# Performance work log

Hardware: AMD Instinct MI355X
Metric: run time of the kernel (lower is better)

The kernel has to match this reference:

```python
import jax, jax.numpy as jnp
import numpy as np
from jax.ops import segment_sum, segment_max

N, E, IN_DIM, HID, HEADS, B, ACTIONS = 16384, 262144, 512, 256, 4, 64, 32
NEG_SLOPE = 0.2  # PyG GATConv default leaky-relu slope


def setup_inputs() -> dict:
    key = jax.random.key(0)
    ks = jax.random.split(key, 12)
    x = jax.random.normal(ks[0], (N, IN_DIM), dtype=jnp.float32)
    edge_index = jax.random.randint(ks[1], (2, E), 0, N, dtype=jnp.int64)
    batch = jnp.sort(jax.random.randint(ks[2], (N,), 0, B, dtype=jnp.int64))
    s = 0.05
    return {
        "x": x,
        "edge_index": edge_index,
        "batch": batch,
        # SAGEConv: lin_l (neighbors, with bias) + lin_r (root, no bias)
        "sage_w_l": jax.random.normal(ks[3], (IN_DIM, HID), dtype=jnp.float32) * s,
        "sage_b_l": jnp.zeros((HID,), dtype=jnp.float32),
        "sage_w_r": jax.random.normal(ks[4], (IN_DIM, HID), dtype=jnp.float32) * s,
        # GATConv: shared lin, per-head attention vectors, output bias (concat=False)
        "gat_w": jax.random.normal(ks[5], (HID, HEADS * HID), dtype=jnp.float32) * s,
        "gat_att_src": jax.random.normal(ks[6], (HEADS, HID), dtype=jnp.float32) * s,
        "gat_att_dst": jax.random.normal(ks[7], (HEADS, HID), dtype=jnp.float32) * s,
        "gat_b": jnp.zeros((HID,), dtype=jnp.float32),
        # action head
        "head_w": jax.random.normal(ks[8], (HID, ACTIONS), dtype=jnp.float32) * s,
        "head_b": jnp.zeros((ACTIONS,), dtype=jnp.float32),
    }


def reference(x, edge_index, batch, sage_w_l, sage_b_l, sage_w_r,
              gat_w, gat_att_src, gat_att_dst, gat_b, head_w, head_b):
    src, dst = edge_index[0], edge_index[1]

    # ---- SAGEConv (mean aggregation): lin_l(mean_j x_j) + lin_r(x_i) ----
    agg = segment_sum(x[src], dst, num_segments=N)                 # [N, IN_DIM]
    deg = segment_sum(jnp.ones((E,), x.dtype), dst, num_segments=N)
    mean_nbr = agg / jnp.maximum(deg, 1.0)[:, None]
    h = mean_nbr @ sage_w_l + sage_b_l + x @ sage_w_r              # [N, HID]
    h = jax.nn.relu(h)
    # dropout is identity at inference (training=False)

    # ---- GATConv (adds self-loops, concat=False -> head average) ----
    loop = jnp.arange(N, dtype=src.dtype)
    si = jnp.concatenate([src, loop])                              # [E2]
    di = jnp.concatenate([dst, loop])
    g = (h @ gat_w).reshape(N, HEADS, HID)                         # [N, H, C]
    a_src = jnp.einsum('nhc,hc->nh', g, gat_att_src)               # [N, H]
    a_dst = jnp.einsum('nhc,hc->nh', g, gat_att_dst)
    logits = jax.nn.leaky_relu(a_src[si] + a_dst[di], NEG_SLOPE)   # [E2, H]
    m = segment_max(logits, di, num_segments=N)                    # per-target max
    ex = jnp.exp(logits - m[di])
    denom = segment_sum(ex, di, num_segments=N)
    alpha = ex / denom[di]                                         # [E2, H]
    out = segment_sum(g[si] * alpha[:, :, None], di, num_segments=N)  # [N, H, C]
    out = jax.nn.relu(out.mean(axis=1) + gat_b)                    # [N, HID]

    # ---- global mean pool + action head ----
    pooled = segment_sum(out, batch, num_segments=B)
    cnt = segment_sum(jnp.ones((N,), out.dtype), batch, num_segments=B)
    pooled = pooled / jnp.maximum(cnt, 1.0)[:, None]               # [B, HID]
    return pooled @ head_w + head_b                                # [B, ACTIONS]
```

## Files before the change

### kernel.cpp

```cpp
#include <hip/hip_runtime.h>
#include <math.h>

#define N_NODES 16384
#define N_EDGES 262144
#define IN_DIM  512
#define HID     256
#define HEADS   4
#define NBATCH  64
#define ACTIONS 32
#define NEG_SLOPE 0.2f

typedef __attribute__((ext_vector_type(8))) short short8;
typedef __attribute__((ext_vector_type(4))) float f32x4;

__device__ __forceinline__ float lrelu(float v) { return v > 0.f ? v : NEG_SLOPE * v; }

__device__ __forceinline__ unsigned short bf16_rne(float f) {
    union { float f; unsigned int u; } x; x.f = f;
    unsigned int u = x.u;
    unsigned int r = (u + 0x7FFFu + ((u >> 16) & 1u)) >> 16;
    return (unsigned short)r;
}

__device__ __forceinline__ float bf16_to_f32(unsigned short s) {
    union { unsigned int u; float f; } x; x.u = (unsigned int)s << 16;
    return x.f;
}

__device__ __forceinline__ float4 bf4_to_f4(ushort4 u) {
    return make_float4(bf16_to_f32(u.x), bf16_to_f32(u.y), bf16_to_f32(u.z), bf16_to_f32(u.w));
}

__device__ __forceinline__ void async_copy16(const unsigned short* g, unsigned short* l) {
    __builtin_amdgcn_global_load_lds(
        (const __attribute__((address_space(1))) unsigned int*)g,
        (__attribute__((address_space(3))) unsigned int*)l, 16, 0, 0);
}

#define NB_WLR   1024
#define NB_WSTK  1024
#define NB_WATT  8
#define NB_DEG   1024
#define NB_XCONV 4096
#define NB_SETUP (NB_WLR + NB_WSTK + NB_WATT + NB_DEG + NB_XCONV)

__global__ __launch_bounds__(256) void setup_kernel(
        const float* __restrict__ wl, const float* __restrict__ wr, unsigned short* __restrict__ bt1,
        const float* __restrict__ gat_w, unsigned short* __restrict__ bt2,
        const float* __restrict__ att_src, const float* __restrict__ att_dst, float* __restrict__ watt,
        const int* __restrict__ ei, int* __restrict__ deg,
        const float* __restrict__ x, unsigned short* __restrict__ xb) {
    int bid = blockIdx.x, tid = threadIdx.x;
    if (bid < NB_WLR) {
        int idx = bid * 256 + tid;
        int j = idx >> 9;
        int k = idx & 511;
        float v = (j < HID) ? wl[k * HID + j] : wr[k * HID + (j - HID)];
        bt1[idx] = bf16_rne(v);
    } else if (bid < NB_WLR + NB_WSTK) {
        int idx = (bid - NB_WLR) * 256 + tid;
        int c = idx >> 10;
        int r = idx & 1023;
        int h = r >> 8;
        int k = r & 255;
        bt2[idx] = bf16_rne(gat_w[(size_t)k * (HEADS * HID) + h * HID + c]);
    } else if (bid < NB_WLR + NB_WSTK + NB_WATT) {
        int j = bid - NB_WLR - NB_WSTK;
        int c = tid;
        int hh = j & 3;
        const float* att = (j < 4) ? (att_src + hh * HID) : (att_dst + hh * HID);
        float s = 0.f;
        for (int cc = 0; cc < HID; cc++)
            s += gat_w[(size_t)c * (HEADS * HID) + hh * HID + cc] * att[cc];
        watt[j * HID + c] = s;
    } else if (bid < NB_WLR + NB_WSTK + NB_WATT + NB_DEG) {
        int e = (bid - NB_WLR - NB_WSTK - NB_WATT) * 256 + tid;
        if (e < N_EDGES) atomicAdd(&deg[ei[N_EDGES + e]], 1);
    } else {
        size_t idx = (size_t)(bid - NB_WLR - NB_WSTK - NB_WATT - NB_DEG) * 2048 + (size_t)tid * 8;
        float4 a0 = *(const float4*)(x + idx);
        float4 a1 = *(const float4*)(x + idx + 4);
        short8 p;
        p[0] = (short)bf16_rne(a0.x); p[1] = (short)bf16_rne(a0.y);
        p[2] = (short)bf16_rne(a0.z); p[3] = (short)bf16_rne(a0.w);
        p[4] = (short)bf16_rne(a1.x); p[5] = (short)bf16_rne(a1.y);
        p[6] = (short)bf16_rne(a1.z); p[7] = (short)bf16_rne(a1.w);
        *(short8*)(xb + idx) = p;
    }
}

__global__ __launch_bounds__(256) void scan_kernel(const int* __restrict__ deg,
                                                   int* __restrict__ row_start,
                                                   int* __restrict__ pos) {
    int t = threadIdx.x;
    int lane = t & 63, wv = t >> 6;
    int base = t * 64;
    int4 buf[16];
    int sum = 0;
#pragma unroll
    for (int i = 0; i < 16; i++) {
        buf[i] = ((const int4*)(deg + base))[i];
        sum += buf[i].x + buf[i].y + buf[i].z + buf[i].w;
    }
    int v = sum;
#pragma unroll
    for (int off = 1; off < 64; off <<= 1) {
        int u = __shfl_up(v, off);
        if (lane >= off) v += u;
    }
    __shared__ int wsum[4];
    if (lane == 63) wsum[wv] = v;
    __syncthreads();
    int wbase = 0;
    for (int w0 = 0; w0 < wv; w0++) wbase += wsum[w0];
    int run = wbase + v - sum;
#pragma unroll
    for (int i = 0; i < 16; i++) {
        int4 b = buf[i];
        int4 o;
        o.x = run; run += b.x;
        o.y = run; run += b.y;
        o.z = run; run += b.z;
        o.w = run; run += b.w;
        ((int4*)(row_start + base))[i] = o;
        ((int4*)(pos + base))[i] = o;
    }
    if (t == 255) row_start[N_NODES] = run;
}

__global__ void fill_kernel(const int* __restrict__ ei, int* __restrict__ pos,
                            int* __restrict__ col) {
    int e = blockIdx.x * 256 + threadIdx.x;
    if (e < N_EDGES) {
        int s = ei[e];
        int d = ei[N_EDGES + e];
        int p = atomicAdd(&pos[d], 1);
        col[p] = s;
    }
}

#define BK 32

__global__ __launch_bounds__(256) void gemm1_kernel(const unsigned short* __restrict__ Ab,
                                                    const unsigned short* __restrict__ Bt,
                                                    unsigned short* __restrict__ Cb,
                                                    int Nn, int K) {
    __shared__ __align__(16) unsigned short As[2][2][64 * BK];
    __shared__ __align__(16) unsigned short Bs[2][2][128 * BK];

    int tid  = threadIdx.x;
    int wv   = tid >> 6;
    int lane = tid & 63;
    int m0 = blockIdx.y * 64;
    int n0 = blockIdx.x * 128;
    int wm = (wv & 1) * 32;
    int wn = (wv >> 1) * 64;

    int srow = tid >> 2;
    int scol = (tid & 3) * 8;
    const unsigned short* Ag  = Ab + (size_t)(m0 + srow) * K + scol;
    const unsigned short* Bg0 = Bt + (size_t)(n0 + srow) * K + scol;
    const unsigned short* Bg1 = Bt + (size_t)(n0 + 64 + srow) * K + scol;

    int fr = lane & 15;
    int fk = (lane >> 4) * 8;
    f32x4 acc[2][4] = {};

#pragma unroll
    for (int s = 0; s < 2; s++) {
        int ko = s * BK;
        async_copy16(Ag + ko,      &As[0][s][wv * 512]);
        async_copy16(Bg0 + ko,     &Bs[0][s][wv * 512]);
        async_copy16(Bg1 + ko,     &Bs[0][s][2048 + wv * 512]);
    }
    __syncthreads();

    int cur = 0;
    for (int kt = 0; kt < K; kt += 2 * BK) {
        int nxt = kt + 2 * BK;
        bool pf = nxt < K;
        if (pf) {
#pragma unroll
            for (int s = 0; s < 2; s++) {
                int ko = nxt + s * BK;
                async_copy16(Ag + ko,  &As[cur ^ 1][s][wv * 512]);
                async_copy16(Bg0 + ko, &Bs[cur ^ 1][s][wv * 512]);
                async_copy16(Bg1 + ko, &Bs[cur ^ 1][s][2048 + wv * 512]);
            }
        }

#pragma unroll
        for (int s = 0; s < 2; s++) {
            short8 af[2], bf[4];
#pragma unroll
            for (int mi = 0; mi < 2; mi++)
                af[mi] = *(const short8*)&As[cur][s][(wm + mi * 16 + fr) * BK + fk];
#pragma unroll
            for (int ni = 0; ni < 4; ni++)
                bf[ni] = *(const short8*)&Bs[cur][s][(wn + ni * 16 + fr) * BK + fk];
#pragma unroll
            for (int mi = 0; mi < 2; mi++)
#pragma unroll
                for (int ni = 0; ni < 4; ni++)
                    acc[mi][ni] = __builtin_amdgcn_mfma_f32_16x16x32_bf16(af[mi], bf[ni], acc[mi][ni], 0, 0, 0);
        }
        __syncthreads();
        cur ^= 1;
    }

    int cr = (lane >> 4) * 4;
    int cc = lane & 15;
#pragma unroll
    for (int mi = 0; mi < 2; mi++) {
#pragma unroll
        for (int ni = 0; ni < 4; ni++) {
            int gc = n0 + wn + ni * 16 + cc;
#pragma unroll
            for (int r = 0; r < 4; r++) {
                int gr = m0 + wm + mi * 16 + cr + r;
                Cb[(size_t)gr * Nn + gc] = bf16_rne(acc[mi][ni][r]);
            }
        }
    }
}

__global__ __launch_bounds__(256) void gemm2_pool_kernel(const unsigned short* __restrict__ A,
                                                         const unsigned short* __restrict__ Bt,
                                                         const int* __restrict__ batch,
                                                         const float* __restrict__ bias,
                                                         float scale,
                                                         float* __restrict__ pooled,
                                                         int Nn, int K) {
    __shared__ __align__(16) unsigned short As[2][2][64 * BK];
    __shared__ __align__(16) unsigned short Bs[2][2][64 * BK];
    __shared__ int bsh[64];

    int tid  = threadIdx.x;
    int wv   = tid >> 6;
    int lane = tid & 63;
    int m0 = blockIdx.y * 64;
    int n0 = blockIdx.x * 64;
    int wm = (wv & 1) * 32;
    int wn = (wv >> 1) * 32;

    if (tid < 64) bsh[tid] = batch[m0 + tid];

    int srow = tid >> 2;
    int scol = (tid & 3) * 8;
    const unsigned short* Ag = A  + (size_t)(m0 + srow) * K + scol;
    const unsigned short* Bg = Bt + (size_t)(n0 + srow) * K + scol;

    int fr = lane & 15;
    int fk = (lane >> 4) * 8;
    f32x4 acc[2][2] = {};

#pragma unroll
    for (int s = 0; s < 2; s++) {
        int ko = s * BK;
        async_copy16(Ag + ko, &As[0][s][wv * 512]);
        async_copy16(Bg + ko, &Bs[0][s][wv * 512]);
    }
    __syncthreads();

    int cur = 0;
    for (int kt = 0; kt < K; kt += 2 * BK) {
        int nxt = kt + 2 * BK;
        bool pf = nxt < K;
        if (pf) {
#pragma unroll
            for (int s = 0; s < 2; s++) {
                int ko = nxt + s * BK;
                async_copy16(Ag + ko, &As[cur ^ 1][s][wv * 512]);
                async_copy16(Bg + ko, &Bs[cur ^ 1][s][wv * 512]);
            }
        }

#pragma unroll
        for (int s = 0; s < 2; s++) {
            short8 af[2], bf[2];
#pragma unroll
            for (int mi = 0; mi < 2; mi++)
                af[mi] = *(const short8*)&As[cur][s][(wm + mi * 16 + fr) * BK + fk];
#pragma unroll
            for (int ni = 0; ni < 2; ni++)
                bf[ni] = *(const short8*)&Bs[cur][s][(wn + ni * 16 + fr) * BK + fk];
#pragma unroll
            for (int mi = 0; mi < 2; mi++)
#pragma unroll
                for (int ni = 0; ni < 2; ni++)
                    acc[mi][ni] = __builtin_amdgcn_mfma_f32_16x16x32_bf16(af[mi], bf[ni], acc[mi][ni], 0, 0, 0);
        }
        __syncthreads();
        cur ^= 1;
    }

    int cr = (lane >> 4) * 4;
    int cc = lane & 15;
#pragma unroll
    for (int mi = 0; mi < 2; mi++) {
        int rowb = wm + mi * 16 + cr;
        int b0 = bsh[rowb], b3 = bsh[rowb + 3];
#pragma unroll
        for (int ni = 0; ni < 2; ni++) {
            int gc = n0 + wn + ni * 16 + cc;
            float b = bias[gc];
            float v0 = fmaxf(fmaf(acc[mi][ni][0], scale, b), 0.f);
            float v1 = fmaxf(fmaf(acc[mi][ni][1], scale, b), 0.f);
            float v2 = fmaxf(fmaf(acc[mi][ni][2], scale, b), 0.f);
            float v3 = fmaxf(fmaf(acc[mi][ni][3], scale, b), 0.f);
            if (b0 == b3) {
                atomicAdd(&pooled[b0 * HID + gc], (v0 + v1) + (v2 + v3));
            } else {
                atomicAdd(&pooled[bsh[rowb + 0] * HID + gc], v0);
                atomicAdd(&pooled[bsh[rowb + 1] * HID + gc], v1);
                atomicAdd(&pooled[bsh[rowb + 2] * HID + gc], v2);
                atomicAdd(&pooled[bsh[rowb + 3] * HID + gc], v3);
            }
        }
    }
}

__global__ __launch_bounds__(256) void sage_agg_kernel(const unsigned short* __restrict__ xlr,
                                                       const int* __restrict__ row_start,
                                                       const int* __restrict__ col,
                                                       const float* __restrict__ b_l,
                                                       const float* __restrict__ watt,
                                                       unsigned short* __restrict__ hb,
                                                       float* __restrict__ a_att) {
    __shared__ float watt_s[8 * HID];
    for (int i = threadIdx.x; i < 8 * HID; i += 256) watt_s[i] = watt[i];
    __syncthreads();

    int wave = threadIdx.x >> 6;
    int lane = threadIdx.x & 63;
    int n = blockIdx.x * 4 + wave;
    int start = row_start[n], end = row_start[n + 1];
    int c0 = lane * 4;

    float4 acc = make_float4(0.f, 0.f, 0.f, 0.f);
    int e = start;
    for (; e + 4 <= end; e += 4) {
        int s0 = col[e], s1 = col[e + 1], s2 = col[e + 2], s3 = col[e + 3];
        ushort4 u0 = *(const ushort4*)(xlr + (size_t)s0 * IN_DIM + c0);
        ushort4 u1 = *(const ushort4*)(xlr + (size_t)s1 * IN_DIM + c0);
        ushort4 u2 = *(const ushort4*)(xlr + (size_t)s2 * IN_DIM + c0);
        ushort4 u3 = *(const ushort4*)(xlr + (size_t)s3 * IN_DIM + c0);
        float4 v0 = bf4_to_f4(u0), v1 = bf4_to_f4(u1), v2 = bf4_to_f4(u2), v3 = bf4_to_f4(u3);
        acc.x += (v0.x + v1.x) + (v2.x + v3.x);
        acc.y += (v0.y + v1.y) + (v2.y + v3.y);
        acc.z += (v0.z + v1.z) + (v2.z + v3.z);
        acc.w += (v0.w + v1.w) + (v2.w + v3.w);
    }
    for (; e < end; e++) {
        int s = col[e];
        float4 v = bf4_to_f4(*(const ushort4*)(xlr + (size_t)s * IN_DIM + c0));
        acc.x += v.x; acc.y += v.y; acc.z += v.z; acc.w += v.w;
    }
    float inv = 1.f / (float)max(end - start, 1);
    float4 xr = bf4_to_f4(*(const ushort4*)(xlr + (size_t)n * IN_DIM + HID + c0));
    float4 bl = *(const float4*)(b_l + c0);
    float4 hv;
    hv.x = fmaxf(fmaf(acc.x, inv, bl.x + xr.x), 0.f);
    hv.y = fmaxf(fmaf(acc.y, inv, bl.y + xr.y), 0.f);
    hv.z = fmaxf(fmaf(acc.z, inv, bl.z + xr.z), 0.f);
    hv.w = fmaxf(fmaf(acc.w, inv, bl.w + xr.w), 0.f);
    ushort4 ho;
    ho.x = bf16_rne(hv.x); ho.y = bf16_rne(hv.y); ho.z = bf16_rne(hv.z); ho.w = bf16_rne(hv.w);
    *(ushort4*)(hb + (size_t)n * HID + c0) = ho;

    float p[8];
#pragma unroll
    for (int j = 0; j < 8; j++) {
        float4 wt = *(const float4*)&watt_s[j * HID + c0];
        p[j] = hv.x * wt.x + hv.y * wt.y + hv.z * wt.z + hv.w * wt.w;
    }
#pragma unroll
    for (int off = 32; off; off >>= 1)
#pragma unroll
        for (int j = 0; j < 8; j++) p[j] += __shfl_down(p[j], off);
    if (lane == 0) {
#pragma unroll
        for (int j = 0; j < 8; j++) a_att[n * 8 + j] = p[j];
    }
}

__global__ __launch_bounds__(256) void gat_agg_kernel(const unsigned short* __restrict__ hb,
                                                      const float* __restrict__ a_att,
                                                      const int* __restrict__ row_start,
                                                      const int* __restrict__ col,
                                                      unsigned short* __restrict__ T) {
    __shared__ __align__(16) float w_s[4][64 * 4];
    int wave = threadIdx.x >> 6;
    int lane = threadIdx.x & 63;
    int n = blockIdx.x * 4 + wave;
    int start = row_start[n], end = row_start[n + 1];

    float4 an = *(const float4*)(a_att + n * 8);
    float4 ad = *(const float4*)(a_att + n * 8 + 4);
    float adst[4] = {ad.x, ad.y, ad.z, ad.w};
    float selfl[4] = {lrelu(an.x + ad.x), lrelu(an.y + ad.y), lrelu(an.z + ad.z), lrelu(an.w + ad.w)};
    float m[4], wself[4];
#pragma unroll
    for (int hh = 0; hh < 4; hh++) {
        m[hh] = fmaxf(selfl[hh], 0.f);
        wself[hh] = __expf(selfl[hh] - m[hh]);
    }

    int c0 = lane * 4;
    float4 hn = bf4_to_f4(*(const ushort4*)(hb + (size_t)n * HID + c0));
    float4 acc[4];
#pragma unroll
    for (int hh = 0; hh < 4; hh++)
        acc[hh] = make_float4(wself[hh] * hn.x, wself[hh] * hn.y, wself[hh] * hn.z, wself[hh] * hn.w);

    float dpart[4] = {0.f, 0.f, 0.f, 0.f};

    for (int base = start; base < end; base += 64) {
        int cnt = min(64, end - base);
        if (lane < cnt) {
            int s = col[base + lane];
            float4 as = *(const float4*)(a_att + s * 8);
            float4 wv;
            wv.x = __expf(lrelu(as.x + adst[0]) - m[0]);
            wv.y = __expf(lrelu(as.y + adst[1]) - m[1]);
            wv.z = __expf(lrelu(as.z + adst[2]) - m[2]);
            wv.w = __expf(lrelu(as.w + adst[3]) - m[3]);
            *(float4*)&w_s[wave][lane * 4] = wv;
            dpart[0] += wv.x; dpart[1] += wv.y; dpart[2] += wv.z; dpart[3] += wv.w;
        }
        __builtin_amdgcn_wave_barrier();

        int i = 0;
        for (; i + 2 <= cnt; i += 2) {
            int s0 = col[base + i], s1 = col[base + i + 1];
            float4 w0 = *(const float4*)&w_s[wave][i * 4];
            float4 w1 = *(const float4*)&w_s[wave][(i + 1) * 4];
            ushort4 u0 = *(const ushort4*)(hb + (size_t)s0 * HID + c0);
            ushort4 u1 = *(const ushort4*)(hb + (size_t)s1 * HID + c0);
            float4 h0 = bf4_to_f4(u0), h1 = bf4_to_f4(u1);
            float wr0[4] = {w0.x, w0.y, w0.z, w0.w};
            float wr1[4] = {w1.x, w1.y, w1.z, w1.w};
#pragma unroll
            for (int hh = 0; hh < 4; hh++) {
                acc[hh].x = fmaf(wr0[hh], h0.x, fmaf(wr1[hh], h1.x, acc[hh].x));
                acc[hh].y = fmaf(wr0[hh], h0.y, fmaf(wr1[hh], h1.y, acc[hh].y));
                acc[hh].z = fmaf(wr0[hh], h0.z, fmaf(wr1[hh], h1.z, acc[hh].z));
                acc[hh].w = fmaf(wr0[hh], h0.w, fmaf(wr1[hh], h1.w, acc[hh].w));
            }
        }
        if (i < cnt) {
            int s0 = col[base + i];
            float4 w0 = *(const float4*)&w_s[wave][i * 4];
            float4 h0 = bf4_to_f4(*(const ushort4*)(hb + (size_t)s0 * HID + c0));
            float wr0[4] = {w0.x, w0.y, w0.z, w0.w};
#pragma unroll
            for (int hh = 0; hh < 4; hh++) {
                acc[hh].x = fmaf(wr0[hh], h0.x, acc[hh].x);
                acc[hh].y = fmaf(wr0[hh], h0.y, acc[hh].y);
                acc[hh].z = fmaf(wr0[hh], h0.z, acc[hh].z);
                acc[hh].w = fmaf(wr0[hh], h0.w, acc[hh].w);
            }
        }
        __builtin_amdgcn_wave_barrier();
    }

#pragma unroll
    for (int off = 32; off; off >>= 1)
#pragma unroll
        for (int hh = 0; hh < 4; hh++) dpart[hh] += __shfl_down(dpart[hh], off);
    float invd[4];
#pragma unroll
    for (int hh = 0; hh < 4; hh++)
        invd[hh] = 1.f / (__shfl(dpart[hh], 0) + wself[hh]);

#pragma unroll
    for (int hh = 0; hh < 4; hh++) {
        ushort4 o;
        o.x = bf16_rne(acc[hh].x * invd[hh]); o.y = bf16_rne(acc[hh].y * invd[hh]);
        o.z = bf16_rne(acc[hh].z * invd[hh]); o.w = bf16_rne(acc[hh].w * invd[hh]);
        *(ushort4*)(T + (size_t)n * (HEADS * HID) + hh * HID + c0) = o;
    }
}

__device__ __forceinline__ int lower_bound_i(const int* a, int n, int v) {
    int lo = 0, hi = n;
    while (lo < hi) {
        int mid = (lo + hi) >> 1;
        if (a[mid] < v) lo = mid + 1; else hi = mid;
    }
    return lo;
}

__global__ __launch_bounds__(256) void head_kernel(const float* __restrict__ pooled,
                                                   const int* __restrict__ batch,
                                                   const float* __restrict__ head_w,
                                                   const float* __restrict__ head_b,
                                                   float* __restrict__ out) {
    __shared__ float sm[HID];
    int b = blockIdx.x;
    int c = threadIdx.x;
    int lo = lower_bound_i(batch, N_NODES, b);
    int hi = lower_bound_i(batch, N_NODES, b + 1);
    int cnt = hi - lo;
    sm[c] = pooled[b * HID + c] / (float)max(cnt, 1);
    __syncthreads();
    if (c < ACTIONS) {
        float acc = head_b[c];
        for (int k = 0; k < HID; k++) acc = fmaf(sm[k], head_w[k * ACTIONS + c], acc);
        out[b * ACTIONS + c] = acc;
    }
}

extern "C" void kernel_launch(void* const* d_in, const int* in_sizes, int n_in,
                              void* d_out, int out_size, void* d_ws, size_t ws_size,
                              hipStream_t stream) {
    const float* x        = (const float*)d_in[0];
    const int*   ei       = (const int*)d_in[1];
    const int*   batch    = (const int*)d_in[2];
    const float* sage_w_l = (const float*)d_in[3];
    const float* sage_b_l = (const float*)d_in[4];
    const float* sage_w_r = (const float*)d_in[5];
    const float* gat_w    = (const float*)d_in[6];
    const float* att_src  = (const float*)d_in[7];
    const float* att_dst  = (const float*)d_in[8];
    const float* gat_b    = (const float*)d_in[9];
    const float* head_w   = (const float*)d_in[10];
    const float* head_b   = (const float*)d_in[11];
    float* out = (float*)d_out;

    char* w = (char*)d_ws;
    int*   deg     = (int*)w;   w += (size_t)N_NODES * 4;
    float* pooled  = (float*)w; w += (size_t)NBATCH * HID * 4;
    size_t zero_bytes = (size_t)N_NODES * 4 + (size_t)NBATCH * HID * 4;
    float* a_att  = (float*)w; w += (size_t)N_NODES * 8 * 4;
    float* watt   = (float*)w; w += (size_t)8 * HID * 4;
    unsigned short* xlr = (unsigned short*)w; w += (size_t)N_NODES * IN_DIM * 2;
    unsigned short* hb  = (unsigned short*)w; w += (size_t)N_NODES * HID * 2;
    unsigned short* T   = (unsigned short*)w; w += (size_t)N_NODES * HEADS * HID * 2;
    unsigned short* bt1 = (unsigned short*)w; w += (size_t)(2 * HID) * IN_DIM * 2;
    unsigned short* bt2 = (unsigned short*)w; w += (size_t)HID * (HEADS * HID) * 2;
    int* row_start= (int*)w;   w += (size_t)(N_NODES + 64) * 4;
    int* pos      = (int*)w;   w += (size_t)N_NODES * 4;
    int* col      = (int*)w;   w += (size_t)N_EDGES * 4;

    unsigned short* xb = T;

    hipMemsetAsync(d_ws, 0, zero_bytes, stream);

    setup_kernel<<<NB_SETUP, 256, 0, stream>>>(sage_w_l, sage_w_r, bt1,
                                               gat_w, bt2, att_src, att_dst, watt,
                                               ei, deg, x, xb);

    scan_kernel<<<1, 256, 0, stream>>>(deg, row_start, pos);
    fill_kernel<<<N_EDGES / 256, 256, 0, stream>>>(ei, pos, col);

    gemm1_kernel<<<dim3((2 * HID) / 128, N_NODES / 64), 256, 0, stream>>>(
        xb, bt1, xlr, 2 * HID, IN_DIM);

    sage_agg_kernel<<<N_NODES / 4, 256, 0, stream>>>(xlr, row_start, col, sage_b_l, watt, hb, a_att);

    gat_agg_kernel<<<N_NODES / 4, 256, 0, stream>>>(hb, a_att, row_start, col, T);

    gemm2_pool_kernel<<<dim3(HID / 64, N_NODES / 64), 256, 0, stream>>>(
        T, bt2, batch, gat_b, 0.25f, pooled, HID, HEADS * HID);

    head_kernel<<<NBATCH, 256, 0, stream>>>(pooled, batch, head_w, head_b, out);
}
```

Baseline: 261.1 us.

## Widen gemm2 N-tile, swizzle GEMM block order, parallelize attention-weight precompute

The attention-vector projection in setup is spread across 512 blocks. Each warp now reduces one output element with a shuffle reduction, instead of 8 blocks running 256-long serial loops. gemm2_pool now uses a 64x128 tile, which halves the number of times the A operand is re-read. Both GEMMs remap the block index so that groups of M-tiles are processed together across all N-tiles, aiming for better L2 reuse. The wider tile raises register and LDS use per block and reduces the number of blocks.

```diff
diff --git a/kernel.cpp b/kernel.cpp
--- a/kernel.cpp
+++ b/kernel.cpp
@@ -39,7 +39,7 @@
 
 #define NB_WLR   1024
 #define NB_WSTK  1024
-#define NB_WATT  8
+#define NB_WATT  512
 #define NB_DEG   1024
 #define NB_XCONV 4096
 #define NB_SETUP (NB_WLR + NB_WSTK + NB_WATT + NB_DEG + NB_XCONV)
@@ -65,14 +65,21 @@
         int k = r & 255;
         bt2[idx] = bf16_rne(gat_w[(size_t)k * (HEADS * HID) + h * HID + c]);
     } else if (bid < NB_WLR + NB_WSTK + NB_WATT) {
-        int j = bid - NB_WLR - NB_WSTK;
-        int c = tid;
+        int t    = (bid - NB_WLR - NB_WSTK) * 4 + (tid >> 6);
+        int lane = tid & 63;
+        int j = t >> 8;
+        int c = t & 255;
         int hh = j & 3;
         const float* att = (j < 4) ? (att_src + hh * HID) : (att_dst + hh * HID);
         float s = 0.f;
-        for (int cc = 0; cc < HID; cc++)
+#pragma unroll
+        for (int it = 0; it < 4; it++) {
+            int cc = lane + it * 64;
             s += gat_w[(size_t)c * (HEADS * HID) + hh * HID + cc] * att[cc];
-        watt[j * HID + c] = s;
+        }
+#pragma unroll
+        for (int off = 32; off; off >>= 1) s += __shfl_down(s, off);
+        if (lane == 0) watt[j * HID + c] = s;
     } else if (bid < NB_WLR + NB_WSTK + NB_WATT + NB_DEG) {
         int e = (bid - NB_WLR - NB_WSTK - NB_WATT) * 256 + tid;
         if (e < N_EDGES) atomicAdd(&deg[ei[N_EDGES + e]], 1);
@@ -151,8 +158,12 @@
     int tid  = threadIdx.x;
     int wv   = tid >> 6;
     int lane = tid & 63;
-    int m0 = blockIdx.y * 64;
-    int n0 = blockIdx.x * 128;
+
+    int L = blockIdx.y * 4 + blockIdx.x;
+    int mt = (L & 7) + (L >> 5) * 8;
+    int nt = (L >> 3) & 3;
+    int m0 = mt * 64;
+    int n0 = nt * 128;
     int wm = (wv & 1) * 32;
     int wn = (wv >> 1) * 64;
 
@@ -232,33 +243,39 @@
                                                          float* __restrict__ pooled,
                                                          int Nn, int K) {
     __shared__ __align__(16) unsigned short As[2][2][64 * BK];
-    __shared__ __align__(16) unsigned short Bs[2][2][64 * BK];
+    __shared__ __align__(16) unsigned short Bs[2][2][128 * BK];
     __shared__ int bsh[64];
 
     int tid  = threadIdx.x;
     int wv   = tid >> 6;
     int lane = tid & 63;
-    int m0 = blockIdx.y * 64;
-    int n0 = blockIdx.x * 64;
+
+    int L = blockIdx.y * 2 + blockIdx.x;
+    int mt = (L & 7) + (L >> 4) * 8;
+    int nt = (L >> 3) & 1;
+    int m0 = mt * 64;
+    int n0 = nt * 128;
     int wm = (wv & 1) * 32;
-    int wn = (wv >> 1) * 32;
+    int wn = (wv >> 1) * 64;
 
     if (tid < 64) bsh[tid] = batch[m0 + tid];
 
     int srow = tid >> 2;
     int scol = (tid & 3) * 8;
-    const unsigned short* Ag = A  + (size_t)(m0 + srow) * K + scol;
-    const unsigned short* Bg = Bt + (size_t)(n0 + srow) * K + scol;
+    const unsigned short* Ag  = A  + (size_t)(m0 + srow) * K + scol;
+    const unsigned short* Bg0 = Bt + (size_t)(n0 + srow) * K + scol;
+    const unsigned short* Bg1 = Bt + (size_t)(n0 + 64 + srow) * K + scol;
 
     int fr = lane & 15;
     int fk = (lane >> 4) * 8;
-    f32x4 acc[2][2] = {};
+    f32x4 acc[2][4] = {};
 
 #pragma unroll
     for (int s = 0; s < 2; s++) {
         int ko = s * BK;
-        async_copy16(Ag + ko, &As[0][s][wv * 512]);
-        async_copy16(Bg + ko, &Bs[0][s][wv * 512]);
+        async_copy16(Ag + ko,  &As[0][s][wv * 512]);
+        async_copy16(Bg0 + ko, &Bs[0][s][wv * 512]);
+        async_copy16(Bg1 + ko, &Bs[0][s][2048 + wv * 512]);
     }
     __syncthreads();
 
@@ -270,24 +287,25 @@
 #pragma unroll
             for (int s = 0; s < 2; s++) {
                 int ko = nxt + s * BK;
-                async_copy16(Ag + ko, &As[cur ^ 1][s][wv * 512]);
-                async_copy16(Bg + ko, &Bs[cur ^ 1][s][wv * 512]);
+                async_copy16(Ag + ko,  &As[cur ^ 1][s][wv * 512]);
+                async_copy16(Bg0 + ko, &Bs[cur ^ 1][s][wv * 512]);
+                async_copy16(Bg1 + ko, &Bs[cur ^ 1][s][2048 + wv * 512]);
             }
         }
 
 #pragma unroll
         for (int s = 0; s < 2; s++) {
-            short8 af[2], bf[2];
+            short8 af[2], bf[4];
 #pragma unroll
             for (int mi = 0; mi < 2; mi++)
                 af[mi] = *(const short8*)&As[cur][s][(wm + mi * 16 + fr) * BK + fk];
 #pragma unroll
-            for (int ni = 0; ni < 2; ni++)
+            for (int ni = 0; ni < 4; ni++)
                 bf[ni] = *(const short8*)&Bs[cur][s][(wn + ni * 16 + fr) * BK + fk];
 #pragma unroll
             for (int mi = 0; mi < 2; mi++)
 #pragma unroll
-                for (int ni = 0; ni < 2; ni++)
+                for (int ni = 0; ni < 4; ni++)
                     acc[mi][ni] = __builtin_amdgcn_mfma_f32_16x16x32_bf16(af[mi], bf[ni], acc[mi][ni], 0, 0, 0);
         }
         __syncthreads();
@@ -301,7 +319,7 @@
         int rowb = wm + mi * 16 + cr;
         int b0 = bsh[rowb], b3 = bsh[rowb + 3];
 #pragma unroll
-        for (int ni = 0; ni < 2; ni++) {
+        for (int ni = 0; ni < 4; ni++) {
             int gc = n0 + wn + ni * 16 + cc;
             float b = bias[gc];
             float v0 = fmaxf(fmaf(acc[mi][ni][0], scale, b), 0.f);
@@ -554,14 +572,14 @@
     scan_kernel<<<1, 256, 0, stream>>>(deg, row_start, pos);
     fill_kernel<<<N_EDGES / 256, 256, 0, stream>>>(ei, pos, col);
 
-    gemm1_kernel<<<dim3((2 * HID) / 128, N_NODES / 64), 256, 0, stream>>>(
+    gemm1_kernel<<<dim3(4, N_NODES / 64), 256, 0, stream>>>(
         xb, bt1, xlr, 2 * HID, IN_DIM);
 
     sage_agg_kernel<<<N_NODES / 4, 256, 0, stream>>>(xlr, row_start, col, sage_b_l, watt, hb, a_att);
 
     gat_agg_kernel<<<N_NODES / 4, 256, 0, stream>>>(hb, a_att, row_start, col, T);
 
-    gemm2_pool_kernel<<<dim3(HID / 64, N_NODES / 64), 256, 0, stream>>>(
+    gemm2_pool_kernel<<<dim3(2, N_NODES / 64), 256, 0, stream>>>(
         T, bt2, batch, gat_b, 0.25f, pooled, HID, HEADS * HID);
 
     head_kernel<<<NBATCH, 256, 0, stream>>>(pooled, batch, head_w, head_b, out);
```

Result: faster. 244.6 us (-6.3%).
